# Performance work log

Hardware: AMD Instinct MI355X
Metric: run time of the kernel (lower is better)

## Reference

```python
import jax, jax.numpy as jnp
import numpy as np

MUL = 256            # multiplicity of each irrep block
S = MUL              # scalar (0e) block width
V = MUL * 3          # vector (1e) block width
D = S + V            # total feature width = 1024
N = 32768            # number of nodes
INV3 = 1.0 / np.sqrt(3.0)   # w3j(1,1,0) and w3j(0,1,1) coefficient
INV6 = 1.0 / np.sqrt(6.0)   # w3j(1,1,1) (Levi-Civita) coefficient
A0 = np.sqrt(1.0 / 5.0)     # path weight for 0e outputs: sqrt(dim_out / n_paths) = sqrt(1/5)
A1 = np.sqrt(3.0 / 5.0)     # path weight for 1e outputs: sqrt(3/5)


def _split(x):
    # x: [N, D] -> scalars [N, MUL], vectors [N, MUL, 3]
    return x[:, :S], x[:, S:].reshape(x.shape[0], MUL, 3)


def norm_gate(x, w1, b1, w2, b2):
    # NormGate: gates = MLP([scalars, |vectors|]); out = [gates_s, vectors * gates_v]
    s, v = _split(x)
    nv = jnp.sqrt(jnp.sum(v * v, axis=-1) + 1e-12)           # [N, MUL] per-irrep norms
    f0 = jnp.concatenate([s, nv], axis=-1)                    # [N, 2*MUL]
    g = jax.nn.silu(f0 @ w1 + b1) @ w2 + b2                   # [N, 2*MUL]
    gated = v * g[:, S:, None]                                # ElementwiseTensorProduct with 0e gates
    return jnp.concatenate([g[:, :S], gated.reshape(-1, V)], axis=-1)


def irrep_linear(x, w0, b0, w1):
    # e3nn o3.Linear: per-l multiplicity mixing with 1/sqrt(fan_in) normalization; bias only on 0e
    s, v = _split(x)
    so = s @ (w0 / np.sqrt(MUL)) + b0
    vo = jnp.einsum('nui,uw->nwi', v, w1 / np.sqrt(MUL))
    return jnp.concatenate([so, vo.reshape(-1, V)], axis=-1)


def tensor_product(x1, x2, w):
    # 'uuu' CG tensor product, 5 instructions: (0,0)->0, (0,1)->1, (1,0)->1, (1,1)->0, (1,1)->1
    # w: [5, MUL] per-path per-u learned weights
    s1, v1 = _split(x1)
    s2, v2 = _split(x2)
    out0 = A0 * (w[0] * s1 * s2 + w[3] * INV3 * jnp.sum(v1 * v2, axis=-1))   # [N, MUL]
    out1 = A1 * (INV3 * (w[1] * s1)[:, :, None] * v2
                 + INV3 * (w[2] * s2)[:, :, None] * v1
                 + INV6 * w[4][None, :, None] * jnp.cross(v1, v2))           # [N, MUL, 3]
    return jnp.concatenate([out0, out1.reshape(-1, V)], axis=-1)


def setup_inputs() -> dict:
    key = jax.random.key(0)
    ks = jax.random.split(key, 32)
    d = {}
    d['x'] = jax.random.normal(ks[0], (N, D), dtype=jnp.float32)
    d['old_fii'] = jax.random.normal(ks[1], (N, D), dtype=jnp.float32)
    i = 2
    for pre in ('ng1', 'ng2', 'ngo'):
        d[pre + '_w1'] = jax.random.normal(ks[i], (2 * MUL, 2 * MUL), dtype=jnp.float32) / np.sqrt(2 * MUL); i += 1
        d[pre + '_b1'] = jax.random.normal(ks[i], (2 * MUL,), dtype=jnp.float32) * 0.01; i += 1
        d[pre + '_w2'] = jax.random.normal(ks[i], (2 * MUL, 2 * MUL), dtype=jnp.float32) / np.sqrt(2 * MUL); i += 1
        d[pre + '_b2'] = jax.random.normal(ks[i], (2 * MUL,), dtype=jnp.float32) * 0.01; i += 1
    for pre in ('lin1', 'lin2', 'lin3'):
        d[pre + '_w0'] = jax.random.normal(ks[i], (MUL, MUL), dtype=jnp.float32); i += 1
        d[pre + '_b0'] = jax.random.normal(ks[i], (MUL,), dtype=jnp.float32) * 0.01; i += 1
        d[pre + '_w1'] = jax.random.normal(ks[i], (MUL, MUL), dtype=jnp.float32); i += 1
    d['tp_w'] = jax.random.normal(ks[i], (5, MUL), dtype=jnp.float32)
    return d


def reference(x, old_fii,
              ng1_w1, ng1_b1, ng1_w2, ng1_b2,
              ng2_w1, ng2_b1, ng2_w2, ng2_b2,
              ngo_w1, ngo_b1, ngo_w2, ngo_b2,
              lin1_w0, lin1_b0, lin1_w1,
              lin2_w0, lin2_b0, lin2_w1,
              lin3_w0, lin3_b0, lin3_w1,
              tp_w):
    xl = irrep_linear(norm_gate(x, ng1_w1, ng1_b1, ng1_w2, ng1_b2), lin1_w0, lin1_b0, lin1_w1)
    xr = irrep_linear(norm_gate(x, ng2_w1, ng2_b1, ng2_w2, ng2_b2), lin2_w0, lin2_b0, lin2_w1)
    t = tensor_product(xl, xr, tp_w) + x        # resnet (dims match)
    t = irrep_linear(norm_gate(t, ngo_w1, ngo_b1, ngo_w2, ngo_b2), lin3_w0, lin3_b0, lin3_w1)
    return old_fii + t
```

## Files before the change

### kernel.cpp

```cpp
#include <hip/hip_runtime.h>
#include <stdint.h>
#include <math.h>

typedef unsigned short u16;
typedef __attribute__((ext_vector_type(8))) short short8;
typedef __attribute__((ext_vector_type(4))) float f32x4;

#define A0C 0.44721359549995793f
#define A1C 0.77459666924148340f
#define INV3C 0.57735026918962584f
#define INV6C 0.40824829046386302f

__device__ __forceinline__ float bf2f(u16 u) {
    unsigned v = ((unsigned)u) << 16; float f; __builtin_memcpy(&f, &v, 4); return f;
}
__device__ __forceinline__ u16 f2bf(float f) {
    unsigned u; __builtin_memcpy(&u, &f, 4);
    u += 0x7fffu + ((u >> 16) & 1u);
    return (u16)(u >> 16);
}

__device__ __forceinline__ void gload_lds16(const void* g, void* l) {
    __builtin_amdgcn_global_load_lds((const __attribute__((address_space(1))) unsigned*)g,
                                     (__attribute__((address_space(3))) unsigned*)l, 16, 0, 0);
}

struct WDesc { const float* s; u16* d; int n; float sc; };
struct WArgs { WDesc w[12]; };

__global__ void cvt_weights(WArgs args) {
    WDesc wd = args.w[blockIdx.z];
    int n = wd.n;
    int x0 = blockIdx.x * 32, y0 = blockIdx.y * 32;
    if (x0 >= n || y0 >= n) return;
    __shared__ float tile[32][33];
    int tx = threadIdx.x, ty = threadIdx.y;
#pragma unroll
    for (int j = 0; j < 4; j++)
        tile[ty + 8 * j][tx] = wd.s[(size_t)(y0 + ty + 8 * j) * n + x0 + tx];
    __syncthreads();
#pragma unroll
    for (int j = 0; j < 4; j++)
        wd.d[(size_t)(x0 + ty + 8 * j) * n + y0 + tx] = f2bf(tile[tx][ty + 8 * j] * wd.sc);
}

struct BDesc { const float* s; float* d; int n; };
struct BArgs { BDesc b[9]; };
__global__ void pack_bias(BArgs a) {
    BDesc b = a.b[blockIdx.x];
    for (int i = threadIdx.x; i < b.n; i += 256) b.d[i] = b.s[i];
}

__global__ void prep_f0(const float* __restrict__ x, u16* __restrict__ f0,
                        u16* __restrict__ xv, long ps) {
    __shared__ float row[1024];
    int n = blockIdx.x, u = threadIdx.x;
    const float4* xr = (const float4*)(x + (size_t)n * 1024);
    float4 v4 = xr[u];
    row[4 * u] = v4.x; row[4 * u + 1] = v4.y; row[4 * u + 2] = v4.z; row[4 * u + 3] = v4.w;
    __syncthreads();
    float s = row[u];
    float v0 = row[256 + 3 * u], v1 = row[256 + 3 * u + 1], v2 = row[256 + 3 * u + 2];
    float nv = sqrtf(v0 * v0 + v1 * v1 + v2 * v2 + 1e-12f);
    size_t o = (size_t)n * 256 + u;
    f0[(size_t)n * 512 + u] = f2bf(s);
    f0[(size_t)n * 512 + 256 + u] = f2bf(nv);
    xv[o] = f2bf(v0);
    xv[ps + o] = f2bf(v1);
    xv[2 * ps + o] = f2bf(v2);
}

__global__ __launch_bounds__(512, 2)
void gemm256(const u16* __restrict__ Ap, int lda, long az,
             const u16* __restrict__ xsrc,
             const u16* __restrict__ gp, int gld, long gz,
             const u16* __restrict__ Bt, long bz,
             const float* __restrict__ bias, int bsz,
             u16* __restrict__ C, int ldc, long czs, long czp,
             int K, long nc, int mode, int act, int nshift)
{
    extern __shared__ __align__(16) u16 sm[];
    u16* As = sm;
    u16* Bs = sm + 32768;

    const int tid = threadIdx.x;
    const int lane = tid & 63;
    const int wid = tid >> 6;
    const int wr = wid >> 2, wc = wid & 3;
    const int lr = lane & 15, hk = lane >> 4;

    int nwg = gridDim.x;
    int lid = blockIdx.x;
    int wg;
    if ((nwg & 7) == 0) { int q = nwg >> 3; wg = (lid & 7) * q + (lid >> 3); }
    else wg = lid;
    const long row0 = (long)(wg >> nshift) * 256;
    const int n0 = (wg & ((1 << nshift) - 1)) * 256;
    const int zi = blockIdx.y;

    long p = 0, rr0 = row0;
    if (mode == 2) { p = row0 / nc; rr0 = row0 - p * nc; }

    const u16* Bz = Bt + (size_t)zi * bz;
    const long cbase = (mode == 2) ? (zi * czs + p * czp + rr0 * ldc)
                                   : (zi * czs + row0 * ldc);

    f32x4 acc[8][4];
#pragma unroll
    for (int m = 0; m < 8; m++)
#pragma unroll
        for (int n = 0; n < 4; n++) acc[m][n] = (f32x4){0.f, 0.f, 0.f, 0.f};

    auto stageB = [&](int buf, int kt) {
#pragma unroll
        for (int it = 0; it < 4; ++it) {
            int idx = it * 512 + tid;
            int r = idx >> 3, s = idx & 7;
            const u16* g = Bz + (size_t)(n0 + r) * K + kt + ((s ^ (r & 7)) * 8);
            u16* l = Bs + buf * 16384 + (size_t)(it * 512 + (tid & 0x1C0)) * 8;
            gload_lds16(g, l);
        }
    };
    auto stageA0 = [&](int buf, int kt) {
#pragma unroll
        for (int it = 0; it < 4; ++it) {
            int idx = it * 512 + tid;
            int r = idx >> 3, s = idx & 7;
            const u16* g = Ap + (size_t)zi * az + (row0 + r) * (size_t)lda + kt + ((s ^ (r & 7)) * 8);
            u16* l = As + buf * 16384 + (size_t)(it * 512 + (tid & 0x1C0)) * 8;
            gload_lds16(g, l);
        }
    };
    auto stageA2 = [&](int buf, int kt) {
#pragma unroll
        for (int it = 0; it < 4; ++it) {
            int idx = it * 512 + tid;
            int r = idx >> 3, s = idx & 7;
            int u = kt + s * 8;
            union { short8 v; u16 h[8]; } gg, tu, pk;
            gg.v = *(const short8*)(gp + (size_t)zi * gz + (rr0 + r) * (size_t)gld + 256 + u);
            tu.v = *(const short8*)(xsrc + (row0 + r) * 256 + u);
#pragma unroll
            for (int j = 0; j < 8; j++) pk.h[j] = f2bf(bf2f(tu.h[j]) * bf2f(gg.h[j]));
            *(short8*)&As[buf * 16384 + ((size_t)r * 8 + (s ^ (r & 7))) * 8] = pk.v;
        }
    };

    const int nt = K >> 6;
    stageB(0, 0);
    if (mode == 0) stageA0(0, 0); else stageA2(0, 0);
    __syncthreads();

    int buf = 0;
    for (int t = 0; t < nt; ++t) {
        if (t + 1 < nt) {
            int kt = (t + 1) << 6;
            stageB(buf ^ 1, kt);
            if (mode == 0) stageA0(buf ^ 1, kt); else stageA2(buf ^ 1, kt);
        }
        const int ao = buf * 16384, bo = buf * 16384;
#pragma unroll
        for (int kk = 0; kk < 2; ++kk) {
            short8 b[4];
#pragma unroll
            for (int n = 0; n < 4; n++) {
                int cb = wc * 64 + n * 16 + lr;
                int sl = (kk * 4 + hk) ^ (cb & 7);
                b[n] = *(const short8*)&Bs[bo + (size_t)cb * 64 + sl * 8];
            }
#pragma unroll
            for (int m = 0; m < 8; m++) {
                int ra = wr * 128 + m * 16 + lr;
                int sl = (kk * 4 + hk) ^ (ra & 7);
                short8 a = *(const short8*)&As[ao + (size_t)ra * 64 + sl * 8];
#pragma unroll
                for (int n = 0; n < 4; n++)
                    acc[m][n] = __builtin_amdgcn_mfma_f32_16x16x32_bf16(a, b[n], acc[m][n], 0, 0, 0);
            }
        }
        __syncthreads();
        buf ^= 1;
    }

#pragma unroll
    for (int n = 0; n < 4; n++) {
        int col = n0 + wc * 64 + n * 16 + lr;
        float bv = (bias && mode == 0) ? bias[(size_t)zi * bsz + col] : 0.0f;
#pragma unroll
        for (int m = 0; m < 8; m++) {
#pragma unroll
            for (int j = 0; j < 4; j++) {
                long rit = wr * 128 + m * 16 + hk * 4 + j;
                float v = acc[m][n][j] + bv;
                if (act) v = v * (1.0f / (1.0f + __expf(-v)));
                C[cbase + rit * (size_t)ldc + col] = f2bf(v);
            }
        }
    }
}

__global__ void tp_res(const u16* __restrict__ xl, const u16* xr_,
                       const float* __restrict__ tpw, const u16* __restrict__ xv,
                       u16* f0, u16* tv, long ps)
{
    int n = blockIdx.x, u = threadIdx.x;
    size_t o = (size_t)n * 256 + u;
    float s1 = bf2f(xl[o]);
    float a1x = bf2f(xl[ps + o]), a1y = bf2f(xl[2 * ps + o]), a1z = bf2f(xl[3 * ps + o]);
    float s2 = bf2f(xr_[o]);
    float b1x = bf2f(xr_[ps + o]), b1y = bf2f(xr_[2 * ps + o]), b1z = bf2f(xr_[3 * ps + o]);
    float xs = bf2f(f0[(size_t)n * 512 + u]);
    float rx = bf2f(xv[o]), ry = bf2f(xv[ps + o]), rz = bf2f(xv[2 * ps + o]);
    float w0 = tpw[u], w1 = tpw[256 + u], w2 = tpw[512 + u], w3 = tpw[768 + u], w4 = tpw[1024 + u];

    float dot = a1x * b1x + a1y * b1y + a1z * b1z;
    float cx = a1y * b1z - a1z * b1y;
    float cy = a1z * b1x - a1x * b1z;
    float cz = a1x * b1y - a1y * b1x;

    float out0 = A0C * (w0 * s1 * s2 + w3 * INV3C * dot) + xs;
    float ox = A1C * (INV3C * (w1 * s1 * b1x + w2 * s2 * a1x) + INV6C * w4 * cx) + rx;
    float oy = A1C * (INV3C * (w1 * s1 * b1y + w2 * s2 * a1y) + INV6C * w4 * cy) + ry;
    float oz = A1C * (INV3C * (w1 * s1 * b1z + w2 * s2 * a1z) + INV6C * w4 * cz) + rz;

    float nv = sqrtf(ox * ox + oy * oy + oz * oz + 1e-12f);
    f0[(size_t)n * 512 + u] = f2bf(out0);
    f0[(size_t)n * 512 + 256 + u] = f2bf(nv);
    tv[o] = f2bf(ox);
    tv[ps + o] = f2bf(oy);
    tv[2 * ps + o] = f2bf(oz);
}

__global__ void repack(const u16* __restrict__ outp, const float* __restrict__ old,
                       float* __restrict__ out, long ps)
{
    __shared__ float add[1024];
    int n = blockIdx.x, u = threadIdx.x;
    size_t o = (size_t)n * 256 + u;
    add[u] = bf2f(outp[o]);
    float vx = bf2f(outp[ps + o]);
    float vy = bf2f(outp[2 * ps + o]);
    float vz = bf2f(outp[3 * ps + o]);
    add[256 + 3 * u] = vx;
    add[256 + 3 * u + 1] = vy;
    add[256 + 3 * u + 2] = vz;
    __syncthreads();
    float4 o4 = ((const float4*)(old + (size_t)n * 1024))[u];
    float4 r;
    r.x = o4.x + add[4 * u];
    r.y = o4.y + add[4 * u + 1];
    r.z = o4.z + add[4 * u + 2];
    r.w = o4.w + add[4 * u + 3];
    ((float4*)(out + (size_t)n * 1024))[u] = r;
}

enum {
    OFF_ng12w1 = 0,
    OFF_ng1w2  = 524288,
    OFF_ngow1  = 1048576,
    OFF_ngow2  = 1310720,
    OFF_l12w0  = 1572864,
    OFF_l12w1  = 1703936,
    OFF_l3w0   = 1835008,
    OFF_l3w1   = 1900544
};
#define BIAS_BYTE_OFF 3932160
enum { BOFF_mlp1 = 0, BOFF_mlp2 = 1024, BOFF_ngo1 = 2048, BOFF_ngo2 = 2560,
       BOFF_l12 = 3072, BOFF_l3 = 3584 };

extern "C" void kernel_launch(void* const* d_in, const int* in_sizes, int n_in,
                              void* d_out, int out_size, void* d_ws, size_t ws_size,
                              hipStream_t stream) {
    const float* x      = (const float*)d_in[0];
    const float* oldf   = (const float*)d_in[1];
    const float* ng1_w1 = (const float*)d_in[2];
    const float* ng1_b1 = (const float*)d_in[3];
    const float* ng1_w2 = (const float*)d_in[4];
    const float* ng1_b2 = (const float*)d_in[5];
    const float* ng2_w1 = (const float*)d_in[6];
    const float* ng2_b1 = (const float*)d_in[7];
    const float* ng2_w2 = (const float*)d_in[8];
    const float* ng2_b2 = (const float*)d_in[9];
    const float* ngo_w1 = (const float*)d_in[10];
    const float* ngo_b1 = (const float*)d_in[11];
    const float* ngo_w2 = (const float*)d_in[12];
    const float* ngo_b2 = (const float*)d_in[13];
    const float* l1_w0  = (const float*)d_in[14];
    const float* l1_b0  = (const float*)d_in[15];
    const float* l1_w1  = (const float*)d_in[16];
    const float* l2_w0  = (const float*)d_in[17];
    const float* l2_b0  = (const float*)d_in[18];
    const float* l2_w1  = (const float*)d_in[19];
    const float* l3_w0  = (const float*)d_in[20];
    const float* l3_b0  = (const float*)d_in[21];
    const float* l3_w1  = (const float*)d_in[22];
    const float* tpw    = (const float*)d_in[23];

    u16* wts = (u16*)d_ws;
    char* wsb = (char*)d_ws;
    float* biasf = (float*)(wsb + BIAS_BYTE_OFF);

    WArgs wa;
    wa.w[0]  = { ng1_w1, wts + OFF_ng12w1,          512, 1.0f };
    wa.w[1]  = { ng2_w1, wts + OFF_ng12w1 + 262144, 512, 1.0f };
    wa.w[2]  = { ng1_w2, wts + OFF_ng1w2,           512, 1.0f };
    wa.w[3]  = { ng2_w2, wts + OFF_ng1w2 + 262144,  512, 1.0f };
    wa.w[4]  = { ngo_w1, wts + OFF_ngow1,           512, 1.0f };
    wa.w[5]  = { ngo_w2, wts + OFF_ngow2,           512, 1.0f };
    wa.w[6]  = { l1_w0, wts + OFF_l12w0,            256, 0.0625f };
    wa.w[7]  = { l2_w0, wts + OFF_l12w0 + 65536,    256, 0.0625f };
    wa.w[8]  = { l1_w1, wts + OFF_l12w1,            256, 0.0625f };
    wa.w[9]  = { l2_w1, wts + OFF_l12w1 + 65536,    256, 0.0625f };
    wa.w[10] = { l3_w0, wts + OFF_l3w0,             256, 0.0625f };
    wa.w[11] = { l3_w1, wts + OFF_l3w1,             256, 0.0625f };
    cvt_weights<<<dim3(16, 16, 12), dim3(32, 8), 0, stream>>>(wa);

    BArgs ba;
    ba.b[0] = { ng1_b1, biasf + BOFF_mlp1,       512 };
    ba.b[1] = { ng2_b1, biasf + BOFF_mlp1 + 512, 512 };
    ba.b[2] = { ng1_b2, biasf + BOFF_mlp2,       512 };
    ba.b[3] = { ng2_b2, biasf + BOFF_mlp2 + 512, 512 };
    ba.b[4] = { ngo_b1, biasf + BOFF_ngo1,       512 };
    ba.b[5] = { ngo_b2, biasf + BOFF_ngo2,       512 };
    ba.b[6] = { l1_b0, biasf + BOFF_l12,         256 };
    ba.b[7] = { l2_b0, biasf + BOFF_l12 + 256,   256 };
    ba.b[8] = { l3_b0, biasf + BOFF_l3,          256 };
    pack_bias<<<9, 256, 0, stream>>>(ba);

    long Nn = (long)in_sizes[0] / 1024;

    int c = 1;
    while (c < 256 &&
           ((unsigned long long)(4ULL << 20) + (unsigned long long)(Nn / c) * 10752ULL > (unsigned long long)ws_size
            || (Nn / c) > 16384))
        c <<= 1;
    long Nc = Nn / c;

    u16* F0 = (u16*)(wsb + (4 << 20));
    u16* H  = F0 + (size_t)Nc * 512;
    u16* G  = H + (size_t)Nc * 1024;
    u16* XV = G + (size_t)Nc * 1024;
    u16* XL = XV + (size_t)Nc * 768;
    long ps = Nc * 256;
    u16* XR = XL + 4 * ps;
    u16* TV = XR + ps;
    u16* OUTP = XL;

    dim3 blk(512);
    const size_t SMEM = 131072;
    int mt = (int)(Nc / 256);

    for (int ch = 0; ch < c; ++ch) {
        const float* xk  = x + (size_t)ch * Nc * 1024;
        const float* ok  = oldf + (size_t)ch * Nc * 1024;
        float* outk = (float*)d_out + (size_t)ch * Nc * 1024;

        prep_f0<<<(int)Nc, 256, 0, stream>>>(xk, F0, XV, ps);

        gemm256<<<dim3(mt * 4, 1), blk, SMEM, stream>>>(F0, 512, 0, nullptr, nullptr, 0, 0,
            wts + OFF_ng12w1, 0, biasf + BOFF_mlp1, 0, H, 1024, 0, 0, 512, Nc, 0, 1, 2);
        gemm256<<<dim3(mt * 2, 2), blk, SMEM, stream>>>(H, 1024, 512, nullptr, nullptr, 0, 0,
            wts + OFF_ng1w2, 262144, biasf + BOFF_mlp2, 512, G, 1024, 512, 0, 512, Nc, 0, 0, 1);
        gemm256<<<dim3(mt, 2), blk, SMEM, stream>>>(G, 1024, 512, nullptr, nullptr, 0, 0,
            wts + OFF_l12w0, 65536, biasf + BOFF_l12, 256, XL, 256, 4 * ps, 0, 256, Nc, 0, 0, 0);
        gemm256<<<dim3(mt * 3, 2), blk, SMEM, stream>>>(nullptr, 0, 0, XV, G, 1024, 512,
            wts + OFF_l12w1, 65536, nullptr, 0, XL + ps, 256, 4 * ps, ps, 256, Nc, 2, 0, 0);

        tp_res<<<(int)Nc, 256, 0, stream>>>(XL, XR, tpw, XV, F0, TV, ps);

        gemm256<<<dim3(mt * 2, 1), blk, SMEM, stream>>>(F0, 512, 0, nullptr, nullptr, 0, 0,
            wts + OFF_ngow1, 0, biasf + BOFF_ngo1, 0, H, 512, 0, 0, 512, Nc, 0, 1, 1);
        gemm256<<<dim3(mt * 2, 1), blk, SMEM, stream>>>(H, 512, 0, nullptr, nullptr, 0, 0,
            wts + OFF_ngow2, 0, biasf + BOFF_ngo2, 0, G, 512, 0, 0, 512, Nc, 0, 0, 1);
        gemm256<<<dim3(mt, 1), blk, SMEM, stream>>>(G, 512, 0, nullptr, nullptr, 0, 0,
            wts + OFF_l3w0, 0, biasf + BOFF_l3, 0, OUTP, 256, 0, 0, 256, Nc, 0, 0, 0);
        gemm256<<<dim3(mt * 3, 1), blk, SMEM, stream>>>(nullptr, 0, 0, TV, G, 512, 0,
            wts + OFF_l3w1, 0, nullptr, 0, OUTP + ps, 256, 0, ps, 256, Nc, 2, 0, 0);

        repack<<<(int)Nc, 256, 0, stream>>>(OUTP, ok, outk, ps);
    }
}
```

Measured before the change: 593.6 us.

## Merge scalar and vector irrep-linear GEMMs into one launch and drop chunk cap

The scalar (w0) and vector (w1) irrep-linear GEMMs now run in a single mode-2 launch. Tiles with p==0 load the scalar activations directly and apply the bias, while p>0 tiles form gated vector products and switch to the w1 weights through a new weight offset. This removes two kernel launches per chunk and lets the two halves fill the GPU together. The 16384-row cap on chunk size is also dropped, so all nodes may be processed in one chunk when the workspace allows. That relies on the w1 weights sitting at a fixed offset after w0, and it makes the buffers larger.

```diff
diff --git a/kernel.cpp b/kernel.cpp
--- a/kernel.cpp
+++ b/kernel.cpp
@@ -74,7 +74,7 @@
 void gemm256(const u16* __restrict__ Ap, int lda, long az,
              const u16* __restrict__ xsrc,
              const u16* __restrict__ gp, int gld, long gz,
-             const u16* __restrict__ Bt, long bz,
+             const u16* __restrict__ Bt, long bz, long bw,
              const float* __restrict__ bias, int bsz,
              u16* __restrict__ C, int ldc, long czs, long czp,
              int K, long nc, int mode, int act, int nshift)
@@ -101,7 +101,7 @@
     long p = 0, rr0 = row0;
     if (mode == 2) { p = row0 / nc; rr0 = row0 - p * nc; }
 
-    const u16* Bz = Bt + (size_t)zi * bz;
+    const u16* Bz = Bt + (size_t)zi * bz + ((mode == 2 && p > 0) ? bw : 0);
     const long cbase = (mode == 2) ? (zi * czs + p * czp + rr0 * ldc)
                                    : (zi * czs + row0 * ldc);
 
@@ -126,7 +126,7 @@
         for (int it = 0; it < 4; ++it) {
             int idx = it * 512 + tid;
             int r = idx >> 3, s = idx & 7;
-            const u16* g = Ap + (size_t)zi * az + (row0 + r) * (size_t)lda + kt + ((s ^ (r & 7)) * 8);
+            const u16* g = Ap + (size_t)zi * az + (rr0 + r) * (size_t)lda + kt + ((s ^ (r & 7)) * 8);
             u16* l = As + buf * 16384 + (size_t)(it * 512 + (tid & 0x1C0)) * 8;
             gload_lds16(g, l);
         }
@@ -139,16 +139,17 @@
             int u = kt + s * 8;
             union { short8 v; u16 h[8]; } gg, tu, pk;
             gg.v = *(const short8*)(gp + (size_t)zi * gz + (rr0 + r) * (size_t)gld + 256 + u);
-            tu.v = *(const short8*)(xsrc + (row0 + r) * 256 + u);
+            tu.v = *(const short8*)(xsrc + (size_t)(row0 - nc + r) * 256 + u);
 #pragma unroll
             for (int j = 0; j < 8; j++) pk.h[j] = f2bf(bf2f(tu.h[j]) * bf2f(gg.h[j]));
             *(short8*)&As[buf * 16384 + ((size_t)r * 8 + (s ^ (r & 7))) * 8] = pk.v;
         }
     };
 
+    const bool a_direct = (mode == 0) || (p == 0);
     const int nt = K >> 6;
     stageB(0, 0);
-    if (mode == 0) stageA0(0, 0); else stageA2(0, 0);
+    if (a_direct) stageA0(0, 0); else stageA2(0, 0);
     __syncthreads();
 
     int buf = 0;
@@ -156,7 +157,7 @@
         if (t + 1 < nt) {
             int kt = (t + 1) << 6;
             stageB(buf ^ 1, kt);
-            if (mode == 0) stageA0(buf ^ 1, kt); else stageA2(buf ^ 1, kt);
+            if (a_direct) stageA0(buf ^ 1, kt); else stageA2(buf ^ 1, kt);
         }
         const int ao = buf * 16384, bo = buf * 16384;
 #pragma unroll
@@ -182,10 +183,11 @@
         buf ^= 1;
     }
 
+    const bool use_bias = bias && (mode == 0 || p == 0);
 #pragma unroll
     for (int n = 0; n < 4; n++) {
         int col = n0 + wc * 64 + n * 16 + lr;
-        float bv = (bias && mode == 0) ? bias[(size_t)zi * bsz + col] : 0.0f;
+        float bv = use_bias ? bias[(size_t)zi * bsz + col] : 0.0f;
 #pragma unroll
         for (int m = 0; m < 8; m++) {
 #pragma unroll
@@ -331,8 +333,7 @@
 
     int c = 1;
     while (c < 256 &&
-           ((unsigned long long)(4ULL << 20) + (unsigned long long)(Nn / c) * 10752ULL > (unsigned long long)ws_size
-            || (Nn / c) > 16384))
+           (unsigned long long)(4ULL << 20) + (unsigned long long)(Nn / c) * 10752ULL > (unsigned long long)ws_size)
         c <<= 1;
     long Nc = Nn / c;
 
@@ -358,24 +359,20 @@
         prep_f0<<<(int)Nc, 256, 0, stream>>>(xk, F0, XV, ps);
 
         gemm256<<<dim3(mt * 4, 1), blk, SMEM, stream>>>(F0, 512, 0, nullptr, nullptr, 0, 0,
-            wts + OFF_ng12w1, 0, biasf + BOFF_mlp1, 0, H, 1024, 0, 0, 512, Nc, 0, 1, 2);
+            wts + OFF_ng12w1, 0, 0, biasf + BOFF_mlp1, 0, H, 1024, 0, 0, 512, Nc, 0, 1, 2);
         gemm256<<<dim3(mt * 2, 2), blk, SMEM, stream>>>(H, 1024, 512, nullptr, nullptr, 0, 0,
-            wts + OFF_ng1w2, 262144, biasf + BOFF_mlp2, 512, G, 1024, 512, 0, 512, Nc, 0, 0, 1);
-        gemm256<<<dim3(mt, 2), blk, SMEM, stream>>>(G, 1024, 512, nullptr, nullptr, 0, 0,
-            wts + OFF_l12w0, 65536, biasf + BOFF_l12, 256, XL, 256, 4 * ps, 0, 256, Nc, 0, 0, 0);
-        gemm256<<<dim3(mt * 3, 2), blk, SMEM, stream>>>(nullptr, 0, 0, XV, G, 1024, 512,
-            wts + OFF_l12w1, 65536, nullptr, 0, XL + ps, 256, 4 * ps, ps, 256, Nc, 2, 0, 0);
+            wts + OFF_ng1w2, 262144, 0, biasf + BOFF_mlp2, 512, G, 1024, 512, 0, 512, Nc, 0, 0, 1);
+        gemm256<<<dim3(mt * 4, 2), blk, SMEM, stream>>>(G, 1024, 512, XV, G, 1024, 512,
+            wts + OFF_l12w0, 65536, 131072, biasf + BOFF_l12, 256, XL, 256, 4 * ps, ps, 256, Nc, 2, 0, 0);
 
         tp_res<<<(int)Nc, 256, 0, stream>>>(XL, XR, tpw, XV, F0, TV, ps);
 
         gemm256<<<dim3(mt * 2, 1), blk, SMEM, stream>>>(F0, 512, 0, nullptr, nullptr, 0, 0,
-            wts + OFF_ngow1, 0, biasf + BOFF_ngo1, 0, H, 512, 0, 0, 512, Nc, 0, 1, 1);
+            wts + OFF_ngow1, 0, 0, biasf + BOFF_ngo1, 0, H, 512, 0, 0, 512, Nc, 0, 1, 1);
         gemm256<<<dim3(mt * 2, 1), blk, SMEM, stream>>>(H, 512, 0, nullptr, nullptr, 0, 0,
-            wts + OFF_ngow2, 0, biasf + BOFF_ngo2, 0, G, 512, 0, 0, 512, Nc, 0, 0, 1);
-        gemm256<<<dim3(mt, 1), blk, SMEM, stream>>>(G, 512, 0, nullptr, nullptr, 0, 0,
-            wts + OFF_l3w0, 0, biasf + BOFF_l3, 0, OUTP, 256, 0, 0, 256, Nc, 0, 0, 0);
-        gemm256<<<dim3(mt * 3, 1), blk, SMEM, stream>>>(nullptr, 0, 0, TV, G, 512, 0,
-            wts + OFF_l3w1, 0, nullptr, 0, OUTP + ps, 256, 0, ps, 256, Nc, 2, 0, 0);
+            wts + OFF_ngow2, 0, 0, biasf + BOFF_ngo2, 0, G, 512, 0, 0, 512, Nc, 0, 0, 1);
+        gemm256<<<dim3(mt * 4, 1), blk, SMEM, stream>>>(G, 512, 0, TV, G, 512, 0,
+            wts + OFF_l3w0, 0, 65536, biasf + BOFF_l3, 0, OUTP, 256, 0, ps, 256, Nc, 2, 0, 0);
 
         repack<<<(int)Nc, 256, 0, stream>>>(OUTP, ok, outk, ps);
     }
```

Result: faster. 539.2 us (-9.2%).
